# Kernel tuning notes

Measured on AMD Instinct MI355X. Metric: run time of the kernel, lower is better.

## Reference

```python
import jax, jax.numpy as jnp
import numpy as np

N, S, F, E, H, O, L, FE = 8, 1024, 64, 512, 8, 64, 6, 4
HD = E // H
FF = FE * E


def setup_inputs() -> dict:
    key = jax.random.key(0)
    ks = iter(jax.random.split(key, 40))
    def rn(shape, s=0.02):
        return jax.random.normal(next(ks), shape, jnp.float32) * s
    return {
        'x': jax.random.normal(next(ks), (N, F, S), jnp.float32),
        'W_first': rn((F, E)), 'b_first': jnp.zeros((E,), jnp.float32),
        'pos_emb': rn((S, E)),
        'Wq': rn((L, HD, HD)), 'bq': jnp.zeros((L, HD), jnp.float32),
        'Wk': rn((L, HD, HD)), 'bk': jnp.zeros((L, HD), jnp.float32),
        'Wv': rn((L, HD, HD)), 'bv': jnp.zeros((L, HD), jnp.float32),
        'Wo': rn((L, E, E)), 'bo': jnp.zeros((L, E), jnp.float32),
        'g1': jnp.ones((L, E), jnp.float32), 'be1': jnp.zeros((L, E), jnp.float32),
        'Wf1': rn((L, E, FF)), 'bf1': jnp.zeros((L, FF), jnp.float32),
        'Wf2': rn((L, FF, E)), 'bf2': jnp.zeros((L, E), jnp.float32),
        'g2': jnp.ones((L, E), jnp.float32), 'be2': jnp.zeros((L, E), jnp.float32),
        'Wfin': rn((E, O)), 'bfin': jnp.zeros((O,), jnp.float32),
    }


def layernorm(x, g, b, eps=1e-5):
    m = jnp.mean(x, axis=-1, keepdims=True)
    v = jnp.mean(jnp.square(x - m), axis=-1, keepdims=True)
    return (x - m) * jax.lax.rsqrt(v + eps) * g + b


def reference(x, W_first, b_first, pos_emb, Wq, bq, Wk, bk, Wv, bv, Wo, bo,
              g1, be1, Wf1, bf1, Wf2, bf2, g2, be2, Wfin, bfin):
    # x: (N, F, S) -> (N, S, F)
    h = jax.nn.relu(jnp.einsum('nfs,fe->nse', x, W_first) + b_first) + pos_emb[None]
    scale = E ** 0.5  # note: module scales by sqrt(embed_size), not sqrt(head_dim)
    for i in range(L):
        t = h.reshape(N, S, H, HD)
        q = jnp.einsum('nshd,de->nshe', t, Wq[i]) + bq[i]
        k = jnp.einsum('nshd,de->nshe', t, Wk[i]) + bk[i]
        v = jnp.einsum('nshd,de->nshe', t, Wv[i]) + bv[i]
        energy = jnp.einsum('nqhd,nkhd->nhqk', q, k)  # (N,H,S,S)
        att = jax.nn.softmax(energy / scale, axis=-1)
        o = jnp.einsum('nhqk,nkhd->nqhd', att, v).reshape(N, S, E)
        o = jnp.einsum('nse,ef->nsf', o, Wo[i]) + bo[i]
        hx = layernorm(o + h, g1[i], be1[i])
        ff = jax.nn.relu(jnp.einsum('nse,ef->nsf', hx, Wf1[i]) + bf1[i])
        ff = jnp.einsum('nsf,fe->nse', ff, Wf2[i]) + bf2[i]
        h = layernorm(ff + hx, g2[i], be2[i])
    # Conv1d kernel_size=1 == pointwise linear over channels; output (N, O, S)
    return jnp.einsum('nse,eo->nos', h, Wfin) + bfin[None, :, None]
```

## Files before the change

kernel.cpp:

```cpp
#include <hip/hip_runtime.h>
#include <hip/hip_bf16.h>
#include <math.h>

#define N_ 8
#define S_ 1024
#define F_ 64
#define E_ 512
#define H_ 8
#define O_ 64
#define L_ 6
#define HD_ 64
#define FF_ 2048
#define SCALE_ 0.044194173824159216f
#define LOG2E_ 1.4426950408889634f
#define QSCALE_ (SCALE_ * LOG2E_)

typedef unsigned short u16;
typedef __attribute__((ext_vector_type(4))) unsigned short u16x4;
typedef __attribute__((ext_vector_type(8))) unsigned short u16x8;
typedef __attribute__((ext_vector_type(8))) short short8;
typedef __attribute__((ext_vector_type(4))) float floatx4;

__device__ __forceinline__ u16 f2b(float f) {
    union { float f; unsigned u; } v; v.f = f;
    unsigned u = v.u;
    unsigned r = (u + 0x7FFFu + ((u >> 16) & 1u)) >> 16;
    return (u16)r;
}
__device__ __forceinline__ u16 f2b_fast(float f) {
    union { float f; unsigned u; } v; v.f = f;
    return (u16)((v.u + 0x8000u) >> 16);
}
__device__ __forceinline__ float b2f(u16 h) {
    union { unsigned u; float f; } v; v.u = ((unsigned)h) << 16;
    return v.f;
}

__global__ __launch_bounds__(256) void first_mfma(
    const float* __restrict__ x, const u16* __restrict__ wt,
    const float* __restrict__ bf, const float* __restrict__ pe,
    u16* __restrict__ resb)
{
    __shared__ u16 a_s[128][72];
    int t = threadIdx.x;
    int w = t >> 6, lane = t & 63, quad = lane >> 4, c16 = lane & 15;
    int rowhalf = w >> 1, colhalf = w & 1;
    int col0 = blockIdx.x * 128;
    int row0 = blockIdx.y * 128;
    int n = row0 >> 10, s0 = row0 & 1023;

    const float* xb = x + (size_t)n * F_ * S_ + s0;
    #pragma unroll
    for (int i = 0; i < 8; i++) {
        int pos = (t + i * 256) * 4;
        int f = pos >> 7, sl = pos & 127;
        float4 v = *(const float4*)&xb[(size_t)f * S_ + sl];
        a_s[sl + 0][f] = f2b_fast(v.x);
        a_s[sl + 1][f] = f2b_fast(v.y);
        a_s[sl + 2][f] = f2b_fast(v.z);
        a_s[sl + 3][f] = f2b_fast(v.w);
    }
    __syncthreads();

    floatx4 acc[4][4];
    #pragma unroll
    for (int mt = 0; mt < 4; mt++)
        #pragma unroll
        for (int nt = 0; nt < 4; nt++) acc[mt][nt] = (floatx4){0.f, 0.f, 0.f, 0.f};

    #pragma unroll
    for (int ks = 0; ks < 2; ks++) {
        short8 af[4], bfr[4];
        #pragma unroll
        for (int mt = 0; mt < 4; mt++)
            af[mt] = *(const short8*)&a_s[rowhalf * 64 + mt * 16 + c16][ks * 32 + quad * 8];
        #pragma unroll
        for (int nt = 0; nt < 4; nt++)
            bfr[nt] = *(const short8*)&wt[(size_t)(col0 + colhalf * 64 + nt * 16 + c16) * F_
                                          + ks * 32 + quad * 8];
        #pragma unroll
        for (int mt = 0; mt < 4; mt++)
            #pragma unroll
            for (int nt = 0; nt < 4; nt++)
                acc[mt][nt] = __builtin_amdgcn_mfma_f32_16x16x32_bf16(
                    af[mt], bfr[nt], acc[mt][nt], 0, 0, 0);
    }

    #pragma unroll
    for (int nt = 0; nt < 4; nt++) {
        int col = col0 + colhalf * 64 + nt * 16 + c16;
        float bv = bf[col];
        #pragma unroll
        for (int mt = 0; mt < 4; mt++) {
            #pragma unroll
            for (int r = 0; r < 4; r++) {
                size_t row = (size_t)row0 + rowhalf * 64 + mt * 16 + quad * 4 + r;
                int s = (int)(row & 1023);
                float v = fmaxf(acc[mt][nt][r] + bv, 0.f) + pe[(size_t)s * E_ + col];
                resb[row * E_ + col] = f2b_fast(v);
            }
        }
    }
}

__global__ __launch_bounds__(256) void wcast_t(
    const float* __restrict__ W0, u16* __restrict__ Wt0, int K, int Nc)
{
    __shared__ float tile[32][33];
    int t = threadIdx.x;
    int bx = blockIdx.x, by = blockIdx.y;
    const float* W = W0 + (size_t)blockIdx.z * K * Nc;
    u16* Wt = Wt0 + (size_t)blockIdx.z * K * Nc;
    #pragma unroll
    for (int i = 0; i < 4; i++) {
        int q = t + i * 256; int r = q >> 5, c = q & 31;
        tile[r][c] = W[(size_t)(by * 32 + r) * Nc + bx * 32 + c];
    }
    __syncthreads();
    #pragma unroll
    for (int i = 0; i < 4; i++) {
        int q = t + i * 256; int r = q >> 5, c = q & 31;
        Wt[(size_t)(bx * 32 + r) * K + by * 32 + c] = f2b(tile[c][r]);
    }
}

__global__ __launch_bounds__(256) void qkvw_cast(
    const float* __restrict__ Wq, const float* __restrict__ Wk,
    const float* __restrict__ Wv,
    u16* __restrict__ wqt, u16* __restrict__ wkt, u16* __restrict__ wvt)
{
    int l = blockIdx.x;
    int t = threadIdx.x;
    size_t off = (size_t)l * HD_ * HD_;
    #pragma unroll
    for (int i = 0; i < 16; i++) {
        int idx = t + i * 256;
        int e = idx >> 6, d = idx & 63;
        wqt[off + idx] = f2b(Wq[off + d * HD_ + e]);
        wkt[off + idx] = f2b(Wk[off + d * HD_ + e]);
        wvt[off + idx] = f2b(Wv[off + d * HD_ + e]);
    }
}

__global__ __launch_bounds__(256) void qkv_mfma(
    const u16* __restrict__ hb,
    const u16* __restrict__ wqt, const u16* __restrict__ wkt,
    const u16* __restrict__ wvt,
    const float* __restrict__ bq, const float* __restrict__ bk,
    const float* __restrict__ bv,
    u16* __restrict__ qo, u16* __restrict__ ko, u16* __restrict__ vo)
{
    __shared__ u16 a_s[256][72];
    int t = threadIdx.x;
    int w = t >> 6, lane = t & 63, quad = lane >> 4, c16 = lane & 15;
    size_t row0 = (size_t)blockIdx.x * 256;

    #pragma unroll
    for (int i = 0; i < 8; i++) {
        int q = t + i * 256; int r = q >> 3, c = q & 7;
        *(u16x8*)&a_s[r][c * 8] = *(const u16x8*)&hb[(row0 + r) * HD_ + c * 8];
    }
    __syncthreads();

    short8 af[4][2];
    #pragma unroll
    for (int mt = 0; mt < 4; mt++)
        #pragma unroll
        for (int ks = 0; ks < 2; ks++)
            af[mt][ks] = *(const short8*)&a_s[w * 64 + mt * 16 + c16][ks * 32 + quad * 8];

    const u16* wts[3] = {wqt, wkt, wvt};
    const float* bs[3] = {bq, bk, bv};
    u16* outs[3] = {qo, ko, vo};

    #pragma unroll
    for (int m = 0; m < 3; m++) {
        short8 bfr[4][2];
        #pragma unroll
        for (int nt = 0; nt < 4; nt++)
            #pragma unroll
            for (int ks = 0; ks < 2; ks++)
                bfr[nt][ks] = *(const short8*)&wts[m][(nt * 16 + c16) * HD_ + ks * 32 + quad * 8];
        floatx4 acc[4][4];
        #pragma unroll
        for (int mt = 0; mt < 4; mt++)
            #pragma unroll
            for (int nt = 0; nt < 4; nt++) acc[mt][nt] = (floatx4){0.f, 0.f, 0.f, 0.f};
        #pragma unroll
        for (int ks = 0; ks < 2; ks++)
            #pragma unroll
            for (int mt = 0; mt < 4; mt++)
                #pragma unroll
                for (int nt = 0; nt < 4; nt++)
                    acc[mt][nt] = __builtin_amdgcn_mfma_f32_16x16x32_bf16(
                        af[mt][ks], bfr[nt][ks], acc[mt][nt], 0, 0, 0);
        float osc = (m == 0) ? QSCALE_ : 1.0f;
        #pragma unroll
        for (int nt = 0; nt < 4; nt++) {
            float bv_ = bs[m][nt * 16 + c16];
            #pragma unroll
            for (int mt = 0; mt < 4; mt++)
                #pragma unroll
                for (int r = 0; r < 4; r++)
                    outs[m][(row0 + w * 64 + mt * 16 + quad * 4 + r) * HD_ + nt * 16 + c16] =
                        f2b_fast((acc[mt][nt][r] + bv_) * osc);
        }
    }
}

__global__ __launch_bounds__(256) void vtrans(
    const u16* __restrict__ vb, u16* __restrict__ vt)
{
    int bid = blockIdx.x;
    int st = bid & 15, hh = (bid >> 4) & 7, n = bid >> 7;
    __shared__ u16 tile[64][72];
    int t = threadIdx.x;
    #pragma unroll
    for (int i = 0; i < 2; i++) {
        int q = t + i * 256; int sl = q >> 3, c = q & 7;
        *(u16x8*)&tile[sl][c * 8] =
            *(const u16x8*)&vb[(((size_t)(n * S_ + st * 64 + sl)) * H_ + hh) * 64 + c * 8];
    }
    __syncthreads();
    #pragma unroll
    for (int i = 0; i < 2; i++) {
        int q = t + i * 256; int d = q >> 3, sc = q & 7;
        u16x8 v;
        #pragma unroll
        for (int j = 0; j < 8; j++) v[j] = tile[sc * 8 + j][d];
        *(u16x8*)&vt[((size_t)(n * H_ + hh) * 64 + d) * (size_t)S_ + st * 64 + sc * 8] = v;
    }
}

__global__ __launch_bounds__(256, 2) void attn_mfma(
    const u16* __restrict__ Q, const u16* __restrict__ K,
    const u16* __restrict__ Vt, u16* __restrict__ O)
{
    int bid = blockIdx.x;
    int qt = bid & 7, hh = (bid >> 3) & 7, n = bid >> 6;
    int t = threadIdx.x;
    int w = t >> 6, lane = t & 63, quad = lane >> 4, c16 = lane & 15;

    __shared__ u16 qp_s[128][72];
    __shared__ u16 k_s[64][72];
    __shared__ u16 vt_s[64][72];
    u16 (*p_s)[72] = &qp_s[w * 32];

    const size_t qkbase = (size_t)n * S_ * E_ + hh * 64;
    const size_t vtbase = ((size_t)(n * H_ + hh) * 64) * (size_t)S_;

    #pragma unroll
    for (int i = 0; i < 4; i++) {
        int q = t + i * 256; int r = q >> 3, c = q & 7;
        *(u16x8*)&qp_s[r][c * 8] =
            *(const u16x8*)&Q[qkbase + (size_t)(qt * 128 + r) * E_ + c * 8];
    }
    __syncthreads();

    short8 qf[2][2];
    #pragma unroll
    for (int nq = 0; nq < 2; nq++)
        #pragma unroll
        for (int ks = 0; ks < 2; ks++)
            qf[nq][ks] = *(const short8*)&qp_s[w * 32 + nq * 16 + c16][ks * 32 + quad * 8];

    const short8 ones = {(short)0x3F80, (short)0x3F80, (short)0x3F80, (short)0x3F80,
                         (short)0x3F80, (short)0x3F80, (short)0x3F80, (short)0x3F80};

    floatx4 oaccT[4][2];
    floatx4 lacc[2];
    #pragma unroll
    for (int nq = 0; nq < 2; nq++) {
        lacc[nq] = (floatx4){0.f, 0.f, 0.f, 0.f};
        #pragma unroll
        for (int mt = 0; mt < 4; mt++) oaccT[mt][nq] = (floatx4){0.f, 0.f, 0.f, 0.f};
    }

    int ar = t >> 3, acq = (t & 7) * 8;
    u16x8 pk[2], pv[2];
    #pragma unroll
    for (int i = 0; i < 2; i++) {
        pk[i] = *(const u16x8*)&K[qkbase + (size_t)(ar + i * 32) * E_ + acq];
        pv[i] = *(const u16x8*)&Vt[vtbase + (size_t)(ar + i * 32) * S_ + acq];
    }

    for (int k0 = 0; k0 < S_; k0 += 64) {
        #pragma unroll
        for (int i = 0; i < 2; i++) {
            *(u16x8*)&k_s[ar + i * 32][acq] = pk[i];
            *(u16x8*)&vt_s[ar + i * 32][acq] = pv[i];
        }
        __syncthreads();
        if (k0 + 64 < S_) {
            #pragma unroll
            for (int i = 0; i < 2; i++) {
                pk[i] = *(const u16x8*)&K[qkbase + (size_t)(k0 + 64 + ar + i * 32) * E_ + acq];
                pv[i] = *(const u16x8*)&Vt[vtbase + (size_t)(ar + i * 32) * S_ + k0 + 64 + acq];
            }
        }

        floatx4 st[4][2];
        #pragma unroll
        for (int mt = 0; mt < 4; mt++)
            #pragma unroll
            for (int nq = 0; nq < 2; nq++) st[mt][nq] = (floatx4){0.f, 0.f, 0.f, 0.f};
        #pragma unroll
        for (int ks = 0; ks < 2; ks++) {
            short8 kf[4];
            #pragma unroll
            for (int mt = 0; mt < 4; mt++)
                kf[mt] = *(const short8*)&k_s[mt * 16 + c16][ks * 32 + quad * 8];
            #pragma unroll
            for (int mt = 0; mt < 4; mt++)
                #pragma unroll
                for (int nq = 0; nq < 2; nq++)
                    st[mt][nq] = __builtin_amdgcn_mfma_f32_16x16x32_bf16(
                        kf[mt], qf[nq][ks], st[mt][nq], 0, 0, 0);
        }

        #pragma unroll
        for (int nq = 0; nq < 2; nq++)
            #pragma unroll
            for (int mt = 0; mt < 4; mt++) {
                u16x4 h;
                #pragma unroll
                for (int r = 0; r < 4; r++) h[r] = f2b_fast(exp2f(st[mt][nq][r]));
                *(u16x4*)&p_s[nq * 16 + c16][mt * 16 + quad * 4] = h;
            }

        #pragma unroll
        for (int ks = 0; ks < 2; ks++) {
            short8 pf[2];
            #pragma unroll
            for (int nq = 0; nq < 2; nq++)
                pf[nq] = *(const short8*)&p_s[nq * 16 + c16][ks * 32 + quad * 8];
            short8 vf[4];
            #pragma unroll
            for (int mt = 0; mt < 4; mt++)
                vf[mt] = *(const short8*)&vt_s[mt * 16 + c16][ks * 32 + quad * 8];
            #pragma unroll
            for (int nq = 0; nq < 2; nq++) {
                lacc[nq] = __builtin_amdgcn_mfma_f32_16x16x32_bf16(ones, pf[nq], lacc[nq], 0, 0, 0);
                #pragma unroll
                for (int mt = 0; mt < 4; mt++)
                    oaccT[mt][nq] = __builtin_amdgcn_mfma_f32_16x16x32_bf16(
                        vf[mt], pf[nq], oaccT[mt][nq], 0, 0, 0);
            }
        }
        __syncthreads();
    }

    #pragma unroll
    for (int nq = 0; nq < 2; nq++) {
        float rl = 1.f / lacc[nq][0];
        int s = qt * 128 + w * 32 + nq * 16 + c16;
        size_t base = (size_t)(n * S_ + s) * E_ + hh * 64;
        #pragma unroll
        for (int mt = 0; mt < 4; mt++) {
            u16x4 h;
            #pragma unroll
            for (int r = 0; r < 4; r++) h[r] = f2b_fast(oaccT[mt][nq][r] * rl);
            *(u16x4*)&O[base + mt * 16 + quad * 4] = h;
        }
    }
}

template <int MT, bool RELU, bool HASRES, bool OUTF32, bool OUTBF16>
__global__ __launch_bounds__(256, 2) void gemm_mfma(
    const u16* __restrict__ A, const u16* __restrict__ Bt,
    const float* __restrict__ bias, const u16* __restrict__ resid,
    float* __restrict__ outf, u16* __restrict__ outb, int M, int Nc, int K)
{
    constexpr int MTILES = MT / 32;
    __shared__ u16 a_s[MT][72];
    __shared__ u16 b_s[128][72];
    int t = threadIdx.x;
    int w = t >> 6, lane = t & 63, quad = lane >> 4, c16 = lane & 15;
    int rowhalf = w >> 1, colhalf = w & 1;
    size_t row0 = (size_t)blockIdx.y * MT;
    size_t col0 = (size_t)blockIdx.x * 128;

    floatx4 acc[MTILES][4];
    #pragma unroll
    for (int mt = 0; mt < MTILES; mt++)
        #pragma unroll
        for (int nt = 0; nt < 4; nt++) acc[mt][nt] = (floatx4){0.f, 0.f, 0.f, 0.f};

    int ar = t >> 3, acq = (t & 7) * 8;
    u16x8 pa[MTILES], pb[4];
    #pragma unroll
    for (int i = 0; i < MTILES; i++)
        pa[i] = *(const u16x8*)&A[(row0 + ar + i * 32) * K + acq];
    #pragma unroll
    for (int i = 0; i < 4; i++)
        pb[i] = *(const u16x8*)&Bt[(col0 + ar + i * 32) * K + acq];

    for (int k0 = 0; k0 < K; k0 += 64) {
        #pragma unroll
        for (int i = 0; i < MTILES; i++)
            *(u16x8*)&a_s[ar + i * 32][acq] = pa[i];
        #pragma unroll
        for (int i = 0; i < 4; i++)
            *(u16x8*)&b_s[ar + i * 32][acq] = pb[i];
        __syncthreads();
        if (k0 + 64 < K) {
            #pragma unroll
            for (int i = 0; i < MTILES; i++)
                pa[i] = *(const u16x8*)&A[(row0 + ar + i * 32) * K + k0 + 64 + acq];
            #pragma unroll
            for (int i = 0; i < 4; i++)
                pb[i] = *(const u16x8*)&Bt[(col0 + ar + i * 32) * K + k0 + 64 + acq];
        }
        #pragma unroll
        for (int ks = 0; ks < 2; ks++) {
            short8 af[MTILES], bf[4];
            #pragma unroll
            for (int mt = 0; mt < MTILES; mt++)
                af[mt] = *(const short8*)&a_s[rowhalf * (MT / 2) + mt * 16 + c16][ks * 32 + quad * 8];
            #pragma unroll
            for (int nt = 0; nt < 4; nt++)
                bf[nt] = *(const short8*)&b_s[colhalf * 64 + nt * 16 + c16][ks * 32 + quad * 8];
            #pragma unroll
            for (int mt = 0; mt < MTILES; mt++)
                #pragma unroll
                for (int nt = 0; nt < 4; nt++)
                    acc[mt][nt] = __builtin_amdgcn_mfma_f32_16x16x32_bf16(
                        af[mt], bf[nt], acc[mt][nt], 0, 0, 0);
        }
        __syncthreads();
    }

    #pragma unroll
    for (int nt = 0; nt < 4; nt++) {
        int col = (int)col0 + colhalf * 64 + nt * 16 + c16;
        float bv = bias[col];
        #pragma unroll
        for (int mt = 0; mt < MTILES; mt++) {
            size_t rowb = row0 + rowhalf * (MT / 2) + mt * 16 + quad * 4;
            #pragma unroll
            for (int r = 0; r < 4; r++) {
                size_t row = rowb + r;
                float v = acc[mt][nt][r] + bv;
                if constexpr (HASRES) v += b2f(resid[row * Nc + col]);
                if constexpr (RELU) v = fmaxf(v, 0.f);
                if constexpr (OUTF32) outf[row * Nc + col] = v;
                if constexpr (OUTBF16) outb[row * Nc + col] = f2b_fast(v);
            }
        }
    }
}

__global__ __launch_bounds__(256) void layernorm_k(
    const float* __restrict__ in, const float* __restrict__ g,
    const float* __restrict__ bb, u16* __restrict__ outb)
{
    int row = blockIdx.x;
    int t = threadIdx.x;
    const float* x = in + (size_t)row * E_;
    float x0 = x[t], x1 = x[t + 256];
    float s = x0 + x1;
    #pragma unroll
    for (int off = 32; off; off >>= 1) s += __shfl_down(s, off, 64);
    __shared__ float red[4];
    int wid = t >> 6, lane = t & 63;
    if (lane == 0) red[wid] = s;
    __syncthreads();
    float m = (red[0] + red[1] + red[2] + red[3]) * (1.f / E_);
    float d0 = x0 - m, d1 = x1 - m;
    float sq = d0 * d0 + d1 * d1;
    #pragma unroll
    for (int off = 32; off; off >>= 1) sq += __shfl_down(sq, off, 64);
    __syncthreads();
    if (lane == 0) red[wid] = sq;
    __syncthreads();
    float var = (red[0] + red[1] + red[2] + red[3]) * (1.f / E_);
    float rstd = rsqrtf(var + 1e-5f);
    outb[(size_t)row * E_ + t] = f2b_fast(d0 * rstd * g[t] + bb[t]);
    outb[(size_t)row * E_ + t + 256] = f2b_fast(d1 * rstd * g[t + 256] + bb[t + 256]);
}

__global__ __launch_bounds__(256) void final_mfma(
    const u16* __restrict__ hb, const u16* __restrict__ wft,
    const float* __restrict__ bfin, float* __restrict__ outp)
{
    __shared__ u16 a_s[64][72];
    int t = threadIdx.x;
    int w = t >> 6, lane = t & 63, quad = lane >> 4, c16 = lane & 15;
    size_t row0 = (size_t)blockIdx.x * 64;

    floatx4 acc[4];
    #pragma unroll
    for (int nt = 0; nt < 4; nt++) acc[nt] = (floatx4){0.f, 0.f, 0.f, 0.f};

    int ar = t >> 3, acq = (t & 7) * 8;
    u16x8 pa[2];
    #pragma unroll
    for (int i = 0; i < 2; i++)
        pa[i] = *(const u16x8*)&hb[(row0 + ar + i * 32) * E_ + acq];

    for (int k0 = 0; k0 < E_; k0 += 64) {
        #pragma unroll
        for (int i = 0; i < 2; i++)
            *(u16x8*)&a_s[ar + i * 32][acq] = pa[i];
        __syncthreads();
        if (k0 + 64 < E_) {
            #pragma unroll
            for (int i = 0; i < 2; i++)
                pa[i] = *(const u16x8*)&hb[(row0 + ar + i * 32) * E_ + k0 + 64 + acq];
        }
        #pragma unroll
        for (int ks = 0; ks < 2; ks++) {
            short8 af = *(const short8*)&a_s[w * 16 + c16][ks * 32 + quad * 8];
            #pragma unroll
            for (int nt = 0; nt < 4; nt++) {
                short8 bf = *(const short8*)&wft[(nt * 16 + c16) * E_ + k0 + ks * 32 + quad * 8];
                acc[nt] = __builtin_amdgcn_mfma_f32_16x16x32_bf16(af, bf, acc[nt], 0, 0, 0);
            }
        }
        __syncthreads();
    }

    #pragma unroll
    for (int nt = 0; nt < 4; nt++) {
        int o = nt * 16 + c16;
        float bv = bfin[o];
        #pragma unroll
        for (int r = 0; r < 4; r++) {
            size_t row = row0 + w * 16 + quad * 4 + r;
            int n = (int)(row >> 10), s = (int)(row & 1023);
            outp[((size_t)(n * O_ + o)) * S_ + s] = acc[nt][r] + bv;
        }
    }
}

extern "C" void kernel_launch(void* const* d_in, const int* in_sizes, int n_in,
                              void* d_out, int out_size, void* d_ws, size_t ws_size,
                              hipStream_t stream)
{
    const float* x       = (const float*)d_in[0];
    const float* W_first = (const float*)d_in[1];
    const float* b_first = (const float*)d_in[2];
    const float* pos_emb = (const float*)d_in[3];
    const float* Wq      = (const float*)d_in[4];
    const float* bq      = (const float*)d_in[5];
    const float* Wk      = (const float*)d_in[6];
    const float* bk      = (const float*)d_in[7];
    const float* Wv      = (const float*)d_in[8];
    const float* bv      = (const float*)d_in[9];
    const float* Wo      = (const float*)d_in[10];
    const float* bo      = (const float*)d_in[11];
    const float* g1      = (const float*)d_in[12];
    const float* be1     = (const float*)d_in[13];
    const float* Wf1     = (const float*)d_in[14];
    const float* bf1     = (const float*)d_in[15];
    const float* Wf2     = (const float*)d_in[16];
    const float* bf2     = (const float*)d_in[17];
    const float* g2      = (const float*)d_in[18];
    const float* be2     = (const float*)d_in[19];
    const float* Wfin    = (const float*)d_in[20];
    const float* bfin    = (const float*)d_in[21];
    float* out = (float*)d_out;

    const size_t M4 = (size_t)N_ * S_ * E_;
    float* t1   = (float*)d_ws;
    u16*   resb = (u16*)(t1 + M4);
    u16*   qb   = resb + M4;
    u16*   kb   = qb + M4;
    u16*   vb   = kb + M4;
    u16*   vt   = vb + M4;
    u16*   ob   = vt + M4;
    u16*   ffb  = qb;
    u16*   wot  = ob + M4;
    u16*   wf1t = wot + (size_t)L_ * E_ * E_;
    u16*   wf2t = wf1t + (size_t)L_ * E_ * FF_;
    u16*   wqt  = wf2t + (size_t)L_ * FF_ * E_;
    u16*   wkt  = wqt + (size_t)L_ * HD_ * HD_;
    u16*   wvt  = wkt + (size_t)L_ * HD_ * HD_;
    u16*   wft  = wvt + (size_t)L_ * HD_ * HD_;
    u16*   w1t  = wft + (size_t)O_ * E_;

    const int rows = N_ * S_;

    qkvw_cast<<<L_, 256, 0, stream>>>(Wq, Wk, Wv, wqt, wkt, wvt);
    wcast_t<<<dim3(E_ / 32, F_ / 32, 1), 256, 0, stream>>>(W_first, w1t, F_, E_);
    wcast_t<<<dim3(E_ / 32, E_ / 32, L_), 256, 0, stream>>>(Wo, wot, E_, E_);
    wcast_t<<<dim3(FF_ / 32, E_ / 32, L_), 256, 0, stream>>>(Wf1, wf1t, E_, FF_);
    wcast_t<<<dim3(E_ / 32, FF_ / 32, L_), 256, 0, stream>>>(Wf2, wf2t, FF_, E_);
    wcast_t<<<dim3(O_ / 32, E_ / 32, 1), 256, 0, stream>>>(Wfin, wft, E_, O_);

    first_mfma<<<dim3(E_ / 128, rows / 128), 256, 0, stream>>>(
        x, w1t, b_first, pos_emb, resb);

    for (int i = 0; i < L_; i++) {
        qkv_mfma<<<256, 256, 0, stream>>>(
            resb, wqt + (size_t)i * HD_ * HD_, wkt + (size_t)i * HD_ * HD_,
            wvt + (size_t)i * HD_ * HD_, bq + i * HD_, bk + i * HD_, bv + i * HD_,
            qb, kb, vb);
        vtrans<<<1024, 256, 0, stream>>>(vb, vt);
        attn_mfma<<<512, 256, 0, stream>>>(qb, kb, vt, ob);
        gemm_mfma<64, false, true, true, false><<<dim3(E_ / 128, rows / 64), 256, 0, stream>>>(
            ob, wot + (size_t)i * E_ * E_, bo + i * E_, resb, t1, nullptr, rows, E_, E_);
        layernorm_k<<<rows, 256, 0, stream>>>(t1, g1 + i * E_, be1 + i * E_, resb);
        gemm_mfma<128, true, false, false, true><<<dim3(FF_ / 128, rows / 128), 256, 0, stream>>>(
            resb, wf1t + (size_t)i * E_ * FF_, bf1 + i * FF_, nullptr, nullptr, ffb,
            rows, FF_, E_);
        gemm_mfma<64, false, true, true, false><<<dim3(E_ / 128, rows / 64), 256, 0, stream>>>(
            ffb, wf2t + (size_t)i * FF_ * E_, bf2 + i * E_, resb, t1, nullptr,
            rows, E_, FF_);
        layernorm_k<<<rows, 256, 0, stream>>>(t1, g2 + i * E_, be2 + i * E_, resb);
    }

    final_mfma<<<rows / 64, 256, 0, stream>>>(resb, wft, bfin, out);
}
```

Measured before the change: 1.017 ms.

## Use direct global-to-LDS loads with XOR swizzle and XCD-aware tile remap in GEMMs

Reworks the GEMM kernel so tiles move from global memory straight into shared memory via global_load_lds instead of staging through registers. Shared memory now uses an XOR-swizzled layout to avoid bank conflicts, and block IDs are remapped across the 8 XCDs for better L2 locality. The Wo and FF2 GEMMs change from 64x128 to 128x64 tiles. The register-prefetch overlap is lost, since loads are issued and waited on within the same iteration with no double buffering, which may expose global latency.

Measured after the change: 1.037 ms. No clear change (+2.0%).

```diff
diff --git a/kernel.cpp b/kernel.cpp
--- a/kernel.cpp
+++ b/kernel.cpp
@@ -36,6 +36,12 @@
     return v.f;
 }
 
+__device__ __forceinline__ void gload16(const u16* g, u16* l) {
+    __builtin_amdgcn_global_load_lds(
+        (const __attribute__((address_space(1))) void*)g,
+        (__attribute__((address_space(3))) void*)l, 16, 0, 0);
+}
+
 __global__ __launch_bounds__(256) void first_mfma(
     const float* __restrict__ x, const u16* __restrict__ wt,
     const float* __restrict__ bf, const float* __restrict__ pe,
@@ -365,78 +371,95 @@
     }
 }
 
-template <int MT, bool RELU, bool HASRES, bool OUTF32, bool OUTBF16>
+template <int MT, int NT, bool RELU, bool HASRES, bool OUTF32, bool OUTBF16>
 __global__ __launch_bounds__(256, 2) void gemm_mfma(
     const u16* __restrict__ A, const u16* __restrict__ Bt,
     const float* __restrict__ bias, const u16* __restrict__ resid,
     float* __restrict__ outf, u16* __restrict__ outb, int M, int Nc, int K)
 {
-    constexpr int MTILES = MT / 32;
-    __shared__ u16 a_s[MT][72];
-    __shared__ u16 b_s[128][72];
+    constexpr int MFR = MT / 32;
+    constexpr int NFR = NT / 32;
+    constexpr int AI  = MT / 32;
+    constexpr int BI  = NT / 32;
+    __shared__ u16 a_s[MT * 64];
+    __shared__ u16 b_s[NT * 64];
+
     int t = threadIdx.x;
     int w = t >> 6, lane = t & 63, quad = lane >> 4, c16 = lane & 15;
-    int rowhalf = w >> 1, colhalf = w & 1;
-    size_t row0 = (size_t)blockIdx.y * MT;
-    size_t col0 = (size_t)blockIdx.x * 128;
-
-    floatx4 acc[MTILES][4];
-    #pragma unroll
-    for (int mt = 0; mt < MTILES; mt++)
-        #pragma unroll
-        for (int nt = 0; nt < 4; nt++) acc[mt][nt] = (floatx4){0.f, 0.f, 0.f, 0.f};
-
-    int ar = t >> 3, acq = (t & 7) * 8;
-    u16x8 pa[MTILES], pb[4];
-    #pragma unroll
-    for (int i = 0; i < MTILES; i++)
-        pa[i] = *(const u16x8*)&A[(row0 + ar + i * 32) * K + acq];
-    #pragma unroll
-    for (int i = 0; i < 4; i++)
-        pb[i] = *(const u16x8*)&Bt[(col0 + ar + i * 32) * K + acq];
+    int rw = w >> 1, cw = w & 1;
+
+    int gx = gridDim.x;
+    int nwg = gx * (int)gridDim.y;
+    int lin = (int)blockIdx.y * gx + (int)blockIdx.x;
+    int cpx = nwg >> 3;
+    int id2 = (lin & 7) * cpx + (lin >> 3);
+    int bx = id2 % gx, by = id2 / gx;
+
+    size_t row0 = (size_t)by * MT;
+    size_t col0 = (size_t)bx * NT;
+
+    size_t aoff[AI]; int adst[AI];
+    #pragma unroll
+    for (int i = 0; i < AI; i++) {
+        int p = t + i * 256;
+        int r = p >> 3;
+        int kch = (p & 7) ^ (r & 7);
+        aoff[i] = (row0 + r) * (size_t)K + kch * 8;
+        adst[i] = w * 512 + i * 2048;
+    }
+    size_t boff[BI]; int bdst[BI];
+    #pragma unroll
+    for (int i = 0; i < BI; i++) {
+        int p = t + i * 256;
+        int r = p >> 3;
+        int kch = (p & 7) ^ (r & 7);
+        boff[i] = (col0 + r) * (size_t)K + kch * 8;
+        bdst[i] = w * 512 + i * 2048;
+    }
+
+    floatx4 acc[MFR][NFR];
+    #pragma unroll
+    for (int mt = 0; mt < MFR; mt++)
+        #pragma unroll
+        for (int nt = 0; nt < NFR; nt++) acc[mt][nt] = (floatx4){0.f, 0.f, 0.f, 0.f};
 
     for (int k0 = 0; k0 < K; k0 += 64) {
         #pragma unroll
-        for (int i = 0; i < MTILES; i++)
-            *(u16x8*)&a_s[ar + i * 32][acq] = pa[i];
-        #pragma unroll
-        for (int i = 0; i < 4; i++)
-            *(u16x8*)&b_s[ar + i * 32][acq] = pb[i];
+        for (int i = 0; i < AI; i++) gload16(A + aoff[i] + k0, a_s + adst[i]);
+        #pragma unroll
+        for (int i = 0; i < BI; i++) gload16(Bt + boff[i] + k0, b_s + bdst[i]);
         __syncthreads();
-        if (k0 + 64 < K) {
-            #pragma unroll
-            for (int i = 0; i < MTILES; i++)
-                pa[i] = *(const u16x8*)&A[(row0 + ar + i * 32) * K + k0 + 64 + acq];
-            #pragma unroll
-            for (int i = 0; i < 4; i++)
-                pb[i] = *(const u16x8*)&Bt[(col0 + ar + i * 32) * K + k0 + 64 + acq];
-        }
+
         #pragma unroll
         for (int ks = 0; ks < 2; ks++) {
-            short8 af[MTILES], bf[4];
-            #pragma unroll
-            for (int mt = 0; mt < MTILES; mt++)
-                af[mt] = *(const short8*)&a_s[rowhalf * (MT / 2) + mt * 16 + c16][ks * 32 + quad * 8];
-            #pragma unroll
-            for (int nt = 0; nt < 4; nt++)
-                bf[nt] = *(const short8*)&b_s[colhalf * 64 + nt * 16 + c16][ks * 32 + quad * 8];
-            #pragma unroll
-            for (int mt = 0; mt < MTILES; mt++)
+            short8 af[MFR], bfr[NFR];
+            #pragma unroll
+            for (int mt = 0; mt < MFR; mt++) {
+                int r = rw * (MT / 2) + mt * 16 + c16;
+                af[mt] = *(const short8*)&a_s[r * 64 + (((ks * 4 + quad) ^ (r & 7)) * 8)];
+            }
+            #pragma unroll
+            for (int nt = 0; nt < NFR; nt++) {
+                int r = cw * (NT / 2) + nt * 16 + c16;
+                bfr[nt] = *(const short8*)&b_s[r * 64 + (((ks * 4 + quad) ^ (r & 7)) * 8)];
+            }
+            #pragma unroll
+            for (int mt = 0; mt < MFR; mt++)
                 #pragma unroll
-                for (int nt = 0; nt < 4; nt++)
+                for (int nt = 0; nt < NFR; nt++)
                     acc[mt][nt] = __builtin_amdgcn_mfma_f32_16x16x32_bf16(
-                        af[mt], bf[nt], acc[mt][nt], 0, 0, 0);
+                        af[mt], bfr[nt], acc[mt][nt], 0, 0, 0);
         }
         __syncthreads();
     }
 
     #pragma unroll
-    for (int nt = 0; nt < 4; nt++) {
-        int col = (int)col0 + colhalf * 64 + nt * 16 + c16;
+    for (int nt = 0; nt < NFR; nt++) {
+        int col = (int)col0 + cw * (NT / 2) + nt * 16 + c16;
         float bv = bias[col];
         #pragma unroll
-        for (int mt = 0; mt < MTILES; mt++) {
-            size_t rowb = row0 + rowhalf * (MT / 2) + mt * 16 + quad * 4;
+        for (int mt = 0; mt < MFR; mt++) {
+            size_t rowb = row0 + rw * (MT / 2) + mt * 16 + quad * 4;
             #pragma unroll
             for (int r = 0; r < 4; r++) {
                 size_t row = rowb + r;
@@ -598,13 +621,13 @@
             qb, kb, vb);
         vtrans<<<1024, 256, 0, stream>>>(vb, vt);
         attn_mfma<<<512, 256, 0, stream>>>(qb, kb, vt, ob);
-        gemm_mfma<64, false, true, true, false><<<dim3(E_ / 128, rows / 64), 256, 0, stream>>>(
+        gemm_mfma<128, 64, false, true, true, false><<<dim3(E_ / 64, rows / 128), 256, 0, stream>>>(
             ob, wot + (size_t)i * E_ * E_, bo + i * E_, resb, t1, nullptr, rows, E_, E_);
         layernorm_k<<<rows, 256, 0, stream>>>(t1, g1 + i * E_, be1 + i * E_, resb);
-        gemm_mfma<128, true, false, false, true><<<dim3(FF_ / 128, rows / 128), 256, 0, stream>>>(
+        gemm_mfma<128, 128, true, false, false, true><<<dim3(FF_ / 128, rows / 128), 256, 0, stream>>>(
             resb, wf1t + (size_t)i * E_ * FF_, bf1 + i * FF_, nullptr, nullptr, ffb,
             rows, FF_, E_);
-        gemm_mfma<64, false, true, true, false><<<dim3(E_ / 128, rows / 64), 256, 0, stream>>>(
+        gemm_mfma<128, 64, false, true, true, false><<<dim3(E_ / 64, rows / 128), 256, 0, stream>>>(
             ffb, wf2t + (size_t)i * FF_ * E_, bf2 + i * E_, resb, t1, nullptr,
             rows, E_, FF_);
         layernorm_k<<<rows, 256, 0, stream>>>(t1, g2 + i * E_, be2 + i * E_, resb);
```
